# Optimization experiments

Hardware: AMD Instinct MI355X
Metric: run time of the kernel (lower is better)

The kernel has to match this reference:

```python
import jax, jax.numpy as jnp
import numpy as np

TEMP = 0.5
LAMDA = 1.0
NUM_SLICE = 64
EPS = 1e-20


def _gaussian_kernel(size=11, sigma=1.5):
    coords = np.arange(size, dtype=np.float64) - (size - 1) / 2.0
    g = np.exp(-(coords ** 2) / (2.0 * sigma ** 2))
    g = g / g.sum()
    return jnp.asarray(g, dtype=jnp.float32)


def _ssim(x, y, data_range=1.0, win_size=11, sigma=1.5):
    # x, y: [B, S, H, W]; treat each slice as an independent 1-channel image.
    B, S, H, W = x.shape
    x4 = x.reshape(B * S, 1, H, W)
    y4 = y.reshape(B * S, 1, H, W)
    g = _gaussian_kernel(win_size, sigma)
    kh = g.reshape(1, 1, win_size, 1)
    kw = g.reshape(1, 1, 1, win_size)
    dn = ('NCHW', 'OIHW', 'NCHW')

    def blur(a):
        a = jax.lax.conv_general_dilated(a, kh, (1, 1), 'VALID', dimension_numbers=dn)
        a = jax.lax.conv_general_dilated(a, kw, (1, 1), 'VALID', dimension_numbers=dn)
        return a

    mu1 = blur(x4)
    mu2 = blur(y4)
    mu1_sq = mu1 * mu1
    mu2_sq = mu2 * mu2
    mu1_mu2 = mu1 * mu2
    sigma1_sq = blur(x4 * x4) - mu1_sq
    sigma2_sq = blur(y4 * y4) - mu2_sq
    sigma12 = blur(x4 * y4) - mu1_mu2
    C1 = (0.01 * data_range) ** 2
    C2 = (0.03 * data_range) ** 2
    ssim_map = ((2.0 * mu1_mu2 + C1) * (2.0 * sigma12 + C2)) / (
        (mu1_sq + mu2_sq + C1) * (sigma1_sq + sigma2_sq + C2))
    return jnp.mean(ssim_map)


def _l1(a, b):
    return jnp.mean(jnp.abs(a - b))


def _cumulative_mips(img_fake, target, gumbel, temp):
    # Growing-window gumbel-softmax MIP, computed in a single O(S) pass.
    # softmax over a prefix window is shift-invariant, so subtract the
    # per-pixel global max over the slice axis for stability, then use cumsums.
    y = img_fake + gumbel
    m = jnp.max(y, axis=1, keepdims=True)
    e = jnp.exp((y - m) / temp)                      # unnormalized softmax weights
    num = jnp.cumsum(e * img_fake, axis=1)
    den = jnp.cumsum(e, axis=1)
    pred_c1 = num / den                              # prefix windows [0:idx+1]
    target_c1 = jax.lax.cummax(target, axis=1)

    ef = jnp.flip(e, axis=1)
    xf = jnp.flip(img_fake, axis=1)
    num2 = jnp.cumsum(ef * xf, axis=1)
    den2 = jnp.cumsum(ef, axis=1)
    pred_c2 = num2 / den2                            # suffix windows [S-1-idx:]
    target_c2 = jax.lax.cummax(jnp.flip(target, axis=1), axis=1)
    return pred_c1, target_c1, pred_c2, target_c2


def _forward(img_fake, target, u_noise):
    gumbel = -jnp.log(-jnp.log(u_noise + EPS) + EPS)
    p1, t1, p2, t2 = _cumulative_mips(img_fake, target, gumbel, TEMP)
    loss_lissim = (_l1(img_fake, target) + 1.0 - _ssim(img_fake, target)) * LAMDA
    loss_mip_c1 = (_l1(p1, t1) + 1.0 - _ssim(p1, t1)) * LAMDA
    loss_mip_c2 = (_l1(p2, t2) + 1.0 - _ssim(p2, t2)) * LAMDA
    return loss_lissim + loss_mip_c1 + loss_mip_c2


def setup_inputs() -> dict:
    key = jax.random.key(0)
    k1, k2, k3 = jax.random.split(key, 3)
    shape = (2, NUM_SLICE, 256, 256)
    img_fake = jax.random.uniform(k1, shape, dtype=jnp.float32)
    target = jax.random.uniform(k2, shape, dtype=jnp.float32)
    u_noise = jax.random.uniform(k3, shape, dtype=jnp.float32)
    return {"img_fake": img_fake, "target": target, "u_noise": u_noise}


def reference(img_fake, target, u_noise):
    return _forward(img_fake, target, u_noise)
```

## Files before the change

kernel.cpp:

```cpp
#include <hip/hip_runtime.h>
#include <cmath>
#include <cstring>

#define NUM_S   64
#define IMG_H   256
#define IMG_W   256
#define HWSZ    (IMG_H*IMG_W)
#define BATCH   2
#define NPIX    (BATCH*HWSZ)
#define NEL     (BATCH*NUM_S*HWSZ)
#define NSLICE  (BATCH*NUM_S)
#define VALID   246
#define EPS_F   1e-20f
#define C1_F    1e-4f
#define C2_F    9e-4f
#define RS      264
#define FS      (16*RS)
#define NSLOT_SCAN 2048
#define NSLOT_ALL  8192
#define PTPAD   1024

typedef __fp16 half8  __attribute__((ext_vector_type(8)));
typedef __fp16 fp16x2 __attribute__((ext_vector_type(2)));
using fragC = __attribute__((ext_vector_type(4))) float;

union H8 { half8 v; short s[8]; int i[4]; };
union PK { fp16x2 v; int i; };
union HS { __fp16 f; short s; };

struct GH { short h[11]; };

__device__ inline fp16x2 pkrtz(float a, float b) {
    return __builtin_amdgcn_cvt_pkrtz(a, b);
}
__device__ inline float frcp(float x)  { return __builtin_amdgcn_rcpf(x); }
__device__ inline float flog2(float x) { return __builtin_amdgcn_logf(x); }
__device__ inline float fexp2(float x) { return __builtin_amdgcn_exp2f(x); }

__device__ inline void block_reduce_slot(float v, float* slot) {
    __shared__ float sm[8];
    __syncthreads();
    #pragma unroll
    for (int off = 32; off; off >>= 1) v += __shfl_down(v, off, 64);
    int lane = threadIdx.x & 63, w = threadIdx.x >> 6;
    if (lane == 0) sm[w] = v;
    __syncthreads();
    if (threadIdx.x == 0) {
        float s = 0.f;
        int nw = blockDim.x >> 6;
        for (int i = 0; i < nw; ++i) s += sm[i];
        *slot = s;
    }
}

__global__ __launch_bounds__(256) void scan_kernel(
    const float* __restrict__ img, const float* __restrict__ tgt,
    const float* __restrict__ un,
    unsigned* __restrict__ pt1, unsigned* __restrict__ pt2,
    float* __restrict__ slots)
{
    int tid = blockIdx.x * 256 + threadIdx.x;
    bool bwd = tid >= NPIX;
    int p = bwd ? tid - NPIX : tid;
    int b  = p >> 16;
    int hw = p & (HWSZ - 1);
    int idx  = b * (NUM_S * HWSZ) + hw + (bwd ? (NUM_S - 1) * HWSZ : 0);
    int step = bwd ? -HWSZ : HWSZ;
    unsigned* __restrict__ pt = bwd ? pt2 : pt1;

    float num = 0.f, den = 0.f, tm = -INFINITY;
    float l1x = 0.f, l1p = 0.f;

    float xb[4], ub[4], tb[4];
    #pragma unroll
    for (int j = 0; j < 4; ++j) {
        int id = idx + j * step;
        xb[j] = img[id]; ub[j] = un[id]; tb[j] = tgt[id];
    }

    for (int i = 0; i < NUM_S; i += 4) {
        #pragma unroll
        for (int j = 0; j < 4; ++j) {
            float x = xb[j], u = ub[j], t = tb[j];
            if (i + j + 4 < NUM_S) {
                int id = idx + 4 * step;
                xb[j] = img[id]; ub[j] = un[id]; tb[j] = tgt[id];
            }
            float w = fmaf(flog2(u + EPS_F), -0.6931471805599453f, EPS_F);
            float r = frcp(w);
            float e = fexp2(x * 2.8853900817779268f) * (r * r);
            num = fmaf(e, x, num);
            den += e;
            float pv = num * frcp(den);
            tm = fmaxf(tm, t);
            if (!bwd) l1x += fabsf(x - t);
            l1p += fabsf(pv - tm);
            PK k; k.v = pkrtz(pv, tm);
            pt[idx] = (unsigned)k.i;
            idx += step;
        }
    }
    block_reduce_slot(bwd ? 0.f : l1x, &slots[blockIdx.x]);
    block_reduce_slot(l1p, &slots[1024 + blockIdx.x]);
}

__global__ __launch_bounds__(256) void ssim_kernel(
    const float* __restrict__ img, const float* __restrict__ tgt,
    const unsigned* __restrict__ pt1, const unsigned* __restrict__ pt2,
    GH gh, float* __restrict__ slots)
{
    __shared__ short Vl[5][FS];
    int pair  = blockIdx.z;
    int base  = blockIdx.y * HWSZ;
    int r0    = blockIdx.x * 16;
    int lane  = threadIdx.x & 63;
    int wid   = threadIdx.x >> 6;
    int q     = lane >> 4;
    int n     = lane & 15;

    H8 band;
    #pragma unroll
    for (int j = 0; j < 8; ++j) {
        int kk = q * 8 + j - n;
        short hv = 0;
        #pragma unroll
        for (int w = 0; w < 11; ++w) hv = (kk == w) ? gh.h[w] : hv;
        band.s[j] = hv;
    }

    for (int d = threadIdx.x; d < 320; d += 256) {
        int f = d >> 6, rm = d & 63, r = rm >> 2, cc = rm & 3;
        ((int*)Vl)[f * 2112 + r * 132 + 128 + cc] = 0;
    }

    bool clampR = (r0 == 240);
    const fragC zero = {0.f, 0.f, 0.f, 0.f};

    unsigned ld[32];
    {
        int rowbase = r0 + q * 8;
        if (pair == 0) {
            const float* ia = img + base;
            const float* ib = tgt + base;
            if (!clampR) {
                const float* pa = ia + rowbase * IMG_W + n;
                const float* pb = ib + rowbase * IMG_W + n;
                #pragma unroll
                for (int it = 0; it < 4; ++it)
                    #pragma unroll
                    for (int j = 0; j < 8; ++j) {
                        int o = j * IMG_W + (wid * 4 + it) * 16;
                        PK k; k.v = pkrtz(pa[o], pb[o]);
                        ld[it * 8 + j] = (unsigned)k.i;
                    }
            } else {
                #pragma unroll
                for (int it = 0; it < 4; ++it)
                    #pragma unroll
                    for (int j = 0; j < 8; ++j) {
                        int rr = min(rowbase + j, IMG_H - 1);
                        int o = rr * IMG_W + (wid * 4 + it) * 16 + n;
                        PK k; k.v = pkrtz(ia[o], ib[o]);
                        ld[it * 8 + j] = (unsigned)k.i;
                    }
            }
        } else {
            const unsigned* __restrict__ pp = (pair == 1 ? pt1 : pt2) + base;
            if (!clampR) {
                const unsigned* pb = pp + rowbase * IMG_W + n;
                #pragma unroll
                for (int it = 0; it < 4; ++it)
                    #pragma unroll
                    for (int j = 0; j < 8; ++j)
                        ld[it * 8 + j] = pb[j * IMG_W + (wid * 4 + it) * 16];
            } else {
                #pragma unroll
                for (int it = 0; it < 4; ++it)
                    #pragma unroll
                    for (int j = 0; j < 8; ++j) {
                        int rr = min(rowbase + j, IMG_H - 1);
                        ld[it * 8 + j] = pp[rr * IMG_W + (wid * 4 + it) * 16 + n];
                    }
            }
        }
    }
    #pragma unroll
    for (int it = 0; it < 4; ++it) {
        H8 fX, fY, fXX, fYY, fXY;
        #pragma unroll
        for (int j = 0; j < 4; ++j) {
            unsigned a = ld[it * 8 + 2 * j], b2 = ld[it * 8 + 2 * j + 1];
            fX.i[j] = (int)((a & 0xffffu) | (b2 << 16));
            fY.i[j] = (int)((a >> 16) | (b2 & 0xffff0000u));
        }
        fXX.v = fX.v * fX.v;
        fYY.v = fY.v * fY.v;
        fXY.v = fX.v * fY.v;
        fragC v0 = __builtin_amdgcn_mfma_f32_16x16x32_f16(band.v, fX.v,  zero, 0, 0, 0);
        fragC v1 = __builtin_amdgcn_mfma_f32_16x16x32_f16(band.v, fY.v,  zero, 0, 0, 0);
        fragC v2 = __builtin_amdgcn_mfma_f32_16x16x32_f16(band.v, fXX.v, zero, 0, 0, 0);
        fragC v3 = __builtin_amdgcn_mfma_f32_16x16x32_f16(band.v, fYY.v, zero, 0, 0, 0);
        fragC v4 = __builtin_amdgcn_mfma_f32_16x16x32_f16(band.v, fXY.v, zero, 0, 0, 0);
        int col = (wid * 4 + it) * 16 + n;
        #pragma unroll
        for (int reg = 0; reg < 4; ++reg) {
            int ro = (q * 4 + reg) * RS + col;
            HS cv;
            cv.f = (__fp16)v0[reg]; Vl[0][ro] = cv.s;
            cv.f = (__fp16)v1[reg]; Vl[1][ro] = cv.s;
            cv.f = (__fp16)v2[reg]; Vl[2][ro] = cv.s;
            cv.f = (__fp16)v3[reg]; Vl[3][ro] = cv.s;
            cv.f = (__fp16)v4[reg]; Vl[4][ro] = cv.s;
        }
    }
    __syncthreads();

    float lsum = 0.f;
    for (int it = 0; it < 4; ++it) {
        int c0 = (wid * 4 + it) * 16;
        int so = n * RS + c0 + q * 8;
        so = min(so, FS - 8);
        H8 a0, a1, a2, a3, a4;
        *(int4*)a0.i = *(const int4*)&Vl[0][so];
        *(int4*)a1.i = *(const int4*)&Vl[1][so];
        *(int4*)a2.i = *(const int4*)&Vl[2][so];
        *(int4*)a3.i = *(const int4*)&Vl[3][so];
        *(int4*)a4.i = *(const int4*)&Vl[4][so];
        fragC o0 = __builtin_amdgcn_mfma_f32_16x16x32_f16(a0.v, band.v, zero, 0, 0, 0);
        fragC o1 = __builtin_amdgcn_mfma_f32_16x16x32_f16(a1.v, band.v, zero, 0, 0, 0);
        fragC o2 = __builtin_amdgcn_mfma_f32_16x16x32_f16(a2.v, band.v, zero, 0, 0, 0);
        fragC o3 = __builtin_amdgcn_mfma_f32_16x16x32_f16(a3.v, band.v, zero, 0, 0, 0);
        fragC o4 = __builtin_amdgcn_mfma_f32_16x16x32_f16(a4.v, band.v, zero, 0, 0, 0);
        #pragma unroll
        for (int reg = 0; reg < 4; ++reg) {
            int r = r0 + q * 4 + reg;
            int c = c0 + n;
            if (r < VALID && c < VALID) {
                float m1 = o0[reg], m2 = o1[reg];
                float s11 = o2[reg] - m1 * m1;
                float s22 = o3[reg] - m2 * m2;
                float s12 = o4[reg] - m1 * m2;
                float nv = (2.f * m1 * m2 + C1_F) * (2.f * s12 + C2_F);
                float dv = (m1 * m1 + m2 * m2 + C1_F) * (s11 + s22 + C2_F);
                lsum += nv * frcp(dv);
            }
        }
    }
    block_reduce_slot(lsum,
        &slots[NSLOT_SCAN + pair * 2048 + blockIdx.y * 16 + blockIdx.x]);
}

__global__ void finalize_kernel(const float* __restrict__ slots,
                                float* __restrict__ out) {
    __shared__ double sa[4], sb[4];
    double a = 0.0, bsum = 0.0;
    for (int i = threadIdx.x; i < NSLOT_SCAN; i += 256) a += (double)slots[i];
    for (int i = NSLOT_SCAN + threadIdx.x; i < NSLOT_ALL; i += 256) bsum += (double)slots[i];
    #pragma unroll
    for (int off = 32; off; off >>= 1) {
        a    += __shfl_down(a, off, 64);
        bsum += __shfl_down(bsum, off, 64);
    }
    int lane = threadIdx.x & 63, w = threadIdx.x >> 6;
    if (lane == 0) { sa[w] = a; sb[w] = bsum; }
    __syncthreads();
    if (threadIdx.x == 0) {
        double A = sa[0] + sa[1] + sa[2] + sa[3];
        double B = sb[0] + sb[1] + sb[2] + sb[3];
        out[0] = (float)(3.0 + A / (double)NEL -
                         B / ((double)NSLICE * (double)VALID * (double)VALID));
    }
}

static unsigned short f32_to_f16(float f) {
    unsigned u; memcpy(&u, &f, 4);
    unsigned s = (u >> 16) & 0x8000u;
    int e = (int)((u >> 23) & 0xff) - 127 + 15;
    unsigned m = u & 0x7fffffu;
    unsigned h = s | ((unsigned)e << 10) | (m >> 13);
    unsigned rem = m & 0x1fffu;
    if (rem > 0x1000u || (rem == 0x1000u && (h & 1))) h++;
    return (unsigned short)h;
}
static double f16_to_d(unsigned short h) {
    unsigned e = (h >> 10) & 0x1f, m = h & 0x3ffu;
    return ldexp((double)(m + 1024), (int)e - 25);
}

extern "C" void kernel_launch(void* const* d_in, const int* in_sizes, int n_in,
                              void* d_out, int out_size, void* d_ws, size_t ws_size,
                              hipStream_t stream) {
    const float* img = (const float*)d_in[0];
    const float* tgt = (const float*)d_in[1];
    const float* un  = (const float*)d_in[2];
    float* out = (float*)d_out;

    unsigned* pt1 = (unsigned*)d_ws;
    unsigned* pt2 = pt1 + NEL + PTPAD;
    float* slots = (float*)(pt2 + NEL);

    GH gh;
    {
        double g[11], s = 0.0;
        for (int i = 0; i < 11; ++i) { double d = i - 5; g[i] = exp(-d * d / 4.5); s += g[i]; }
        for (int i = 0; i < 11; ++i) g[i] /= s;
        for (int iter = 0; iter < 3; ++iter) {
            double sb = 0.0;
            unsigned short h[11];
            for (int i = 0; i < 11; ++i) { h[i] = f32_to_f16((float)g[i]); sb += f16_to_d(h[i]); }
            for (int i = 0; i < 11; ++i) { g[i] /= sb; gh.h[i] = (short)h[i]; }
        }
    }

    scan_kernel<<<2 * NPIX / 256, 256, 0, stream>>>(img, tgt, un, pt1, pt2, slots);
    ssim_kernel<<<dim3(16, NSLICE, 3), 256, 0, stream>>>(img, tgt, pt1, pt2, gh, slots);
    finalize_kernel<<<1, 256, 0, stream>>>(slots, out);
}
```

Measured before the change: 216.2 us.

## Pre-pack fp16 image/target in scan, swizzle LDS layout, nontemporal stores

The scan kernel now also writes a packed fp16 (img, target) buffer, so the SSIM kernel reads one 4-byte value per pixel for all three pairs instead of two fp32 loads for pair 0. The LDS staging buffer drops its padded row stride in favour of an XOR swizzle, which shrinks shared memory and removes the pad-zeroing loop. The final reduction reuses that LDS for scratch, and scan stores become nontemporal. The trade-off is an extra 32 MB write pass in scan to save 64 MB of reads in SSIM, and rows 246 to 255 of the column window now rely on the swizzle instead of padding.

Result: faster. 206.2 us (-4.6%).

```diff
diff --git a/kernel.cpp b/kernel.cpp
--- a/kernel.cpp
+++ b/kernel.cpp
@@ -14,8 +14,7 @@
 #define EPS_F   1e-20f
 #define C1_F    1e-4f
 #define C2_F    9e-4f
-#define RS      264
-#define FS      (16*RS)
+#define FSH     4096
 #define NSLOT_SCAN 2048
 #define NSLOT_ALL  8192
 #define PTPAD   1024
@@ -53,11 +52,24 @@
     }
 }
 
+__device__ inline void block_reduce_vl(float v, float* slot, float* sm) {
+    __syncthreads();
+    #pragma unroll
+    for (int off = 32; off; off >>= 1) v += __shfl_down(v, off, 64);
+    int lane = threadIdx.x & 63, w = threadIdx.x >> 6;
+    if (lane == 0) sm[w] = v;
+    __syncthreads();
+    if (threadIdx.x == 0) {
+        float s = sm[0] + sm[1] + sm[2] + sm[3];
+        *slot = s;
+    }
+}
+
 __global__ __launch_bounds__(256) void scan_kernel(
     const float* __restrict__ img, const float* __restrict__ tgt,
     const float* __restrict__ un,
-    unsigned* __restrict__ pt1, unsigned* __restrict__ pt2,
-    float* __restrict__ slots)
+    unsigned* __restrict__ pt0, unsigned* __restrict__ pt1,
+    unsigned* __restrict__ pt2, float* __restrict__ slots)
 {
     int tid = blockIdx.x * 256 + threadIdx.x;
     bool bwd = tid >= NPIX;
@@ -96,7 +108,11 @@
             if (!bwd) l1x += fabsf(x - t);
             l1p += fabsf(pv - tm);
             PK k; k.v = pkrtz(pv, tm);
-            pt[idx] = (unsigned)k.i;
+            if (!bwd) {
+                PK a; a.v = pkrtz(x, t);
+                __builtin_nontemporal_store((unsigned)a.i, &pt0[idx]);
+            }
+            __builtin_nontemporal_store((unsigned)k.i, &pt[idx]);
             idx += step;
         }
     }
@@ -105,11 +121,11 @@
 }
 
 __global__ __launch_bounds__(256) void ssim_kernel(
-    const float* __restrict__ img, const float* __restrict__ tgt,
-    const unsigned* __restrict__ pt1, const unsigned* __restrict__ pt2,
+    const unsigned* __restrict__ pt0, const unsigned* __restrict__ pt1,
+    const unsigned* __restrict__ pt2,
     GH gh, float* __restrict__ slots)
 {
-    __shared__ short Vl[5][FS];
+    __shared__ short Vl[5][FSH];
     int pair  = blockIdx.z;
     int base  = blockIdx.y * HWSZ;
     int r0    = blockIdx.x * 16;
@@ -128,60 +144,29 @@
         band.s[j] = hv;
     }
 
-    for (int d = threadIdx.x; d < 320; d += 256) {
-        int f = d >> 6, rm = d & 63, r = rm >> 2, cc = rm & 3;
-        ((int*)Vl)[f * 2112 + r * 132 + 128 + cc] = 0;
-    }
-
+    const unsigned* __restrict__ pp =
+        (pair == 0 ? pt0 : (pair == 1 ? pt1 : pt2)) + base;
     bool clampR = (r0 == 240);
     const fragC zero = {0.f, 0.f, 0.f, 0.f};
 
     unsigned ld[32];
     {
         int rowbase = r0 + q * 8;
-        if (pair == 0) {
-            const float* ia = img + base;
-            const float* ib = tgt + base;
-            if (!clampR) {
-                const float* pa = ia + rowbase * IMG_W + n;
-                const float* pb = ib + rowbase * IMG_W + n;
+        if (!clampR) {
+            const unsigned* pb = pp + rowbase * IMG_W + n;
+            #pragma unroll
+            for (int it = 0; it < 4; ++it)
                 #pragma unroll
-                for (int it = 0; it < 4; ++it)
-                    #pragma unroll
-                    for (int j = 0; j < 8; ++j) {
-                        int o = j * IMG_W + (wid * 4 + it) * 16;
-                        PK k; k.v = pkrtz(pa[o], pb[o]);
-                        ld[it * 8 + j] = (unsigned)k.i;
-                    }
-            } else {
+                for (int j = 0; j < 8; ++j)
+                    ld[it * 8 + j] = pb[j * IMG_W + (wid * 4 + it) * 16];
+        } else {
+            #pragma unroll
+            for (int it = 0; it < 4; ++it)
                 #pragma unroll
-                for (int it = 0; it < 4; ++it)
-                    #pragma unroll
-                    for (int j = 0; j < 8; ++j) {
-                        int rr = min(rowbase + j, IMG_H - 1);
-                        int o = rr * IMG_W + (wid * 4 + it) * 16 + n;
-                        PK k; k.v = pkrtz(ia[o], ib[o]);
-                        ld[it * 8 + j] = (unsigned)k.i;
-                    }
-            }
-        } else {
-            const unsigned* __restrict__ pp = (pair == 1 ? pt1 : pt2) + base;
-            if (!clampR) {
-                const unsigned* pb = pp + rowbase * IMG_W + n;
-                #pragma unroll
-                for (int it = 0; it < 4; ++it)
-                    #pragma unroll
-                    for (int j = 0; j < 8; ++j)
-                        ld[it * 8 + j] = pb[j * IMG_W + (wid * 4 + it) * 16];
-            } else {
-                #pragma unroll
-                for (int it = 0; it < 4; ++it)
-                    #pragma unroll
-                    for (int j = 0; j < 8; ++j) {
-                        int rr = min(rowbase + j, IMG_H - 1);
-                        ld[it * 8 + j] = pp[rr * IMG_W + (wid * 4 + it) * 16 + n];
-                    }
-            }
+                for (int j = 0; j < 8; ++j) {
+                    int rr = min(rowbase + j, IMG_H - 1);
+                    ld[it * 8 + j] = pp[rr * IMG_W + (wid * 4 + it) * 16 + n];
+                }
         }
     }
     #pragma unroll
@@ -204,7 +189,8 @@
         int col = (wid * 4 + it) * 16 + n;
         #pragma unroll
         for (int reg = 0; reg < 4; ++reg) {
-            int ro = (q * 4 + reg) * RS + col;
+            int r = q * 4 + reg;
+            int ro = (r << 8) + (col ^ ((r & 7) << 3));
             HS cv;
             cv.f = (__fp16)v0[reg]; Vl[0][ro] = cv.s;
             cv.f = (__fp16)v1[reg]; Vl[1][ro] = cv.s;
@@ -218,8 +204,9 @@
     float lsum = 0.f;
     for (int it = 0; it < 4; ++it) {
         int c0 = (wid * 4 + it) * 16;
-        int so = n * RS + c0 + q * 8;
-        so = min(so, FS - 8);
+        int cb = c0 + q * 8;
+        if (cb > 248) cb = 248;
+        int so = (n << 8) + (cb ^ ((n & 7) << 3));
         H8 a0, a1, a2, a3, a4;
         *(int4*)a0.i = *(const int4*)&Vl[0][so];
         *(int4*)a1.i = *(const int4*)&Vl[1][so];
@@ -246,8 +233,9 @@
             }
         }
     }
-    block_reduce_slot(lsum,
-        &slots[NSLOT_SCAN + pair * 2048 + blockIdx.y * 16 + blockIdx.x]);
+    block_reduce_vl(lsum,
+        &slots[NSLOT_SCAN + pair * 2048 + blockIdx.y * 16 + blockIdx.x],
+        (float*)Vl);
 }
 
 __global__ void finalize_kernel(const float* __restrict__ slots,
@@ -295,7 +283,8 @@
     const float* un  = (const float*)d_in[2];
     float* out = (float*)d_out;
 
-    unsigned* pt1 = (unsigned*)d_ws;
+    unsigned* pt0 = (unsigned*)d_ws;
+    unsigned* pt1 = pt0 + NEL + PTPAD;
     unsigned* pt2 = pt1 + NEL + PTPAD;
     float* slots = (float*)(pt2 + NEL);
 
@@ -312,7 +301,7 @@
         }
     }
 
-    scan_kernel<<<2 * NPIX / 256, 256, 0, stream>>>(img, tgt, un, pt1, pt2, slots);
-    ssim_kernel<<<dim3(16, NSLICE, 3), 256, 0, stream>>>(img, tgt, pt1, pt2, gh, slots);
+    scan_kernel<<<2 * NPIX / 256, 256, 0, stream>>>(img, tgt, un, pt0, pt1, pt2, slots);
+    ssim_kernel<<<dim3(16, NSLICE, 3), 256, 0, stream>>>(pt0, pt1, pt2, gh, slots);
     finalize_kernel<<<1, 256, 0, stream>>>(slots, out);
 }
```
